# Performance work log

Measured on AMD Instinct MI355X. Metric: run time of the kernel, lower is better.

## Reference

```python
import jax, jax.numpy as jnp
import numpy as np

# DeepSeek-V2 MLA dims (one tensor-parallel shard of 8)
H = 5120          # hidden size
S = 2048          # seq len
B = 1
NH = 16           # 128 heads / 8 devices
Q_LORA = 1536
KV_LORA = 512
NOPE = 128
ROPE = 64
QK = NOPE + ROPE  # 192 per-head q/k dim
VD = 128          # v head dim
DEVICE_NUM = 8
EPS = 1e-6


def rms_norm(x, w):
    v = jnp.mean(jnp.square(x.astype(jnp.float32)), axis=-1, keepdims=True)
    return (x * jax.lax.rsqrt(v + EPS)).astype(x.dtype) * w


def rope_cos_sin(position_ids, dim=ROPE, base=10000.0):
    inv_freq = 1.0 / (base ** (jnp.arange(0, dim, 2, dtype=jnp.float32) / dim))
    freqs = position_ids.astype(jnp.float32)[..., None] * inv_freq       # [B,S,dim/2]
    emb = jnp.concatenate([freqs, freqs], axis=-1)                        # [B,S,dim]
    return jnp.cos(emb), jnp.sin(emb)


def apply_rope(x, cos, sin):
    # DeepSeek interleaved reorder: view(b,h,s,d//2,2).transpose(-1,-2).reshape
    b, h, s, d = x.shape
    x = x.reshape(b, h, s, d // 2, 2).transpose(0, 1, 2, 4, 3).reshape(b, h, s, d)
    x1, x2 = x[..., : d // 2], x[..., d // 2:]
    rot = jnp.concatenate([-x2, x1], axis=-1)
    return x * cos[:, None] + rot * sin[:, None]


def setup_inputs() -> dict:
    key = jax.random.key(0)
    ks = jax.random.split(key, 8)
    sc = 0.02
    hidden_states = jax.random.normal(ks[0], (B, S, H), dtype=jnp.float32)
    position_ids = jnp.arange(S, dtype=jnp.int64 if jax.config.jax_enable_x64 else jnp.int32)[None, :].repeat(B, 0)
    attention_mask = jnp.triu(jnp.full((S, S), -1e9, dtype=jnp.float32), 1)[None, None]
    return {
        "hidden_states": hidden_states,
        "position_ids": position_ids,
        "attention_mask": attention_mask,
        "ln_w": jnp.ones((H,), jnp.float32),
        "q_a_w": jax.random.normal(ks[1], (Q_LORA, H), jnp.float32) * sc,
        "q_a_ln_w": jnp.ones((Q_LORA,), jnp.float32),
        "q_b_w": jax.random.normal(ks[2], (NH * QK, Q_LORA), jnp.float32) * sc,
        "kv_a_w": jax.random.normal(ks[3], (KV_LORA + ROPE, H), jnp.float32) * sc,
        "kv_a_ln_w": jnp.ones((KV_LORA,), jnp.float32),
        "kv_b_w": jax.random.normal(ks[4], (NH * (NOPE + VD), KV_LORA), jnp.float32) * sc,
        "o_w": jax.random.normal(ks[5], (H, NH * VD), jnp.float32) * sc,
    }


def reference(hidden_states, position_ids, attention_mask, ln_w, q_a_w, q_a_ln_w,
              q_b_w, kv_a_w, kv_a_ln_w, kv_b_w, o_w):
    b, s, _ = hidden_states.shape
    residual = hidden_states * (1.0 / DEVICE_NUM)
    x = rms_norm(hidden_states, ln_w)

    # Q path: low-rank down-proj + RMSNorm + up-proj
    q = rms_norm(x @ q_a_w.T, q_a_ln_w) @ q_b_w.T                # [b,s,NH*QK]
    q = q.reshape(b, s, NH, QK).transpose(0, 2, 1, 3)            # [b,NH,s,QK]
    q_nope, q_pe = q[..., :NOPE], q[..., NOPE:]

    # KV path: compressed latent + shared rope key
    ckv = x @ kv_a_w.T                                           # [b,s,KV_LORA+ROPE]
    c_kv, k_pe = ckv[..., :KV_LORA], ckv[..., KV_LORA:]
    k_pe = k_pe.reshape(b, s, 1, ROPE).transpose(0, 2, 1, 3)     # [b,1,s,ROPE]
    kv = rms_norm(c_kv, kv_a_ln_w) @ kv_b_w.T                    # [b,s,NH*(NOPE+VD)]
    kv = kv.reshape(b, s, NH, NOPE + VD).transpose(0, 2, 1, 3)
    k_nope, v = kv[..., :NOPE], kv[..., NOPE:]

    cos, sin = rope_cos_sin(position_ids)
    q_pe = apply_rope(q_pe, cos, sin)
    k_pe = apply_rope(k_pe, cos, sin)

    k = jnp.concatenate([k_nope, jnp.broadcast_to(k_pe, (b, NH, s, ROPE))], axis=-1)
    qf = jnp.concatenate([q_nope, q_pe], axis=-1)

    scores = jnp.einsum('bhqd,bhkd->bhqk', qf, k) * (1.0 / np.sqrt(QK))
    scores = scores + attention_mask
    probs = jax.nn.softmax(scores, axis=-1)
    attn = jnp.einsum('bhqk,bhkd->bhqd', probs, v)               # [b,NH,s,VD]

    out = attn.transpose(0, 2, 1, 3).reshape(b, s, NH * VD) @ o_w.T
    hidden = residual + out
    return hidden.astype(jnp.float32), k.astype(jnp.float32), v.astype(jnp.float32)
```

## Files before the change

### kernel.cpp

```cpp
#include <hip/hip_runtime.h>
#include <math.h>

typedef unsigned short u16;
typedef unsigned int u32;
typedef __attribute__((ext_vector_type(8))) short short8;
typedef __attribute__((ext_vector_type(4))) float f32x4;

#define NHEADS 16
static const int S      = 2048;
static const int Hd     = 5120;
static const int QLORA  = 1536;
static const int KVLORA = 512;
static const int NQK    = 192;
static const int NVD    = 128;
static const int QDIM   = 3072;
static const int KVDIM  = 4096;
static const int NFUSE  = 2176;

__device__ __forceinline__ u16 f2bf(float f) {
    union { float f; u32 u; } v; v.f = f;
    u32 r = v.u + 0x7FFFu + ((v.u >> 16) & 1u);
    return (u16)(r >> 16);
}
__device__ __forceinline__ float bf2f(u16 h) {
    union { u32 u; float f; } v; v.u = (u32)h << 16; return v.f;
}

__global__ void convert_all_kernel(const float* __restrict__ o_w,
                                   const float* __restrict__ q_a_w,
                                   const float* __restrict__ kv_a_w,
                                   const float* __restrict__ q_b_w,
                                   const float* __restrict__ kv_b_w,
                                   u16* __restrict__ o_wb, u16* __restrict__ Wf,
                                   u16* __restrict__ q_b_wb, u16* __restrict__ kv_b_wb) {
    long c = (long)blockIdx.x * 256 + threadIdx.x;
    const float* src; u16* dst; long nsrcc;
    if (c < 2621440L)      { src = o_w;    dst = o_wb;            nsrcc = 2621440L; }
    else if (c < 4587520L) { c -= 2621440L; src = q_a_w; dst = Wf; nsrcc = 1966080L; }
    else if (c < 5406720L) { c -= 4587520L; src = kv_a_w; dst = Wf + 7864320L; nsrcc = 737280L; }
    else if (c < 6586368L) { c -= 5406720L; src = q_b_w;  dst = q_b_wb;  nsrcc = 1179648L; }
    else if (c < 7110656L) { c -= 6586368L; src = kv_b_w; dst = kv_b_wb; nsrcc = 524288L; }
    else return;
    union { u16 h[4]; uint2 u; } p;
    if (c < nsrcc) {
        float4 v = *(const float4*)(src + c * 4);
        p.h[0] = f2bf(v.x); p.h[1] = f2bf(v.y); p.h[2] = f2bf(v.z); p.h[3] = f2bf(v.w);
    } else {
        p.h[0] = p.h[1] = p.h[2] = p.h[3] = 0;
    }
    *(uint2*)(dst + c * 4) = p.u;
}

__global__ void rmsnorm_bf16_kernel(const float* in, const float* __restrict__ w,
                                    u16* out, int D, int in_stride, int out_stride) {
    int row = blockIdx.x;
    const float* x = in + (size_t)row * in_stride;
    u16* y = out + (size_t)row * out_stride;
    float ss = 0.f;
    for (int i = threadIdx.x; i < D; i += blockDim.x) { float v = x[i]; ss += v * v; }
    #pragma unroll
    for (int off = 32; off > 0; off >>= 1) ss += __shfl_xor(ss, off);
    __shared__ float wsum[8];
    int wid = threadIdx.x >> 6, lane = threadIdx.x & 63;
    if (lane == 0) wsum[wid] = ss;
    __syncthreads();
    float tot = 0.f;
    int nw = blockDim.x >> 6;
    for (int i = 0; i < nw; ++i) tot += wsum[i];
    float scale = rsqrtf(tot / (float)D + 1e-6f);
    for (int i = threadIdx.x; i < D; i += blockDim.x) y[i] = f2bf(x[i] * scale * w[i]);
}

__global__ void rms_qkv_kernel(const u16* __restrict__ CF,
                               const float* __restrict__ qw, const float* __restrict__ kw,
                               u16* __restrict__ QAn, u16* __restrict__ CKVN) {
    const int row = blockIdx.x;
    const u16* x; u16* y; const float* w; int D;
    if (blockIdx.y == 0) {
        x = CF + (size_t)row * NFUSE;          y = QAn + (size_t)row * QLORA;
        w = qw; D = QLORA;
    } else {
        x = CF + (size_t)row * NFUSE + QLORA;  y = CKVN + (size_t)row * KVLORA;
        w = kw; D = KVLORA;
    }
    float ss = 0.f;
    for (int i = threadIdx.x; i < D; i += blockDim.x) { float v = bf2f(x[i]); ss += v * v; }
    #pragma unroll
    for (int off = 32; off > 0; off >>= 1) ss += __shfl_xor(ss, off);
    __shared__ float wsum[4];
    int wid = threadIdx.x >> 6, lane = threadIdx.x & 63;
    if (lane == 0) wsum[wid] = ss;
    __syncthreads();
    float tot = wsum[0] + wsum[1] + wsum[2] + wsum[3];
    float scale = rsqrtf(tot / (float)D + 1e-6f);
    for (int i = threadIdx.x; i < D; i += blockDim.x) y[i] = f2bf(bf2f(x[i]) * scale * w[i]);
}

template<int BM, bool SWZ, bool OBF, bool QPERM>
__global__ __launch_bounds__(256) void gemm_k(
    const u16* __restrict__ A, const u16* __restrict__ B, void* __restrict__ Cv,
    int M, int N, int K, const float* __restrict__ resid) {
    constexpr int MR = BM / 32;
    __shared__ u16 As[4][BM * 32];
    __shared__ u16 Bs[4][128 * 32];

    int bm, bn;
    if constexpr (SWZ) {
        const int lin = blockIdx.x + blockIdx.y * gridDim.x;
        const int nwg = gridDim.x * gridDim.y;
        const int xcd = lin & 7, off = lin >> 3;
        const int q = nwg >> 3, r = nwg & 7;
        const int wg = (xcd < r ? xcd * (q + 1) : r * (q + 1) + (xcd - r) * q) + off;
        bm = (wg % gridDim.y) * BM;
        bn = (wg / gridDim.y) * 128;
    } else {
        bm = blockIdx.y * BM;
        bn = blockIdx.x * 128;
    }

    const int tid = threadIdx.x;
    const int w = tid >> 6, lane = tid & 63;
    const int wr = w >> 1, wc = w & 1;
    const int fr = lane & 15, kg = lane >> 4;

    f32x4 acc[MR][4];
    #pragma unroll
    for (int i = 0; i < MR; ++i)
        #pragma unroll
        for (int j = 0; j < 4; ++j) acc[i][j] = (f32x4){0.f, 0.f, 0.f, 0.f};

    const int srow = lane >> 2;
    const int scol = (lane & 3) * 8;
    const u16* Ap0 = A + (size_t)(bm + w * (BM / 4) + srow) * K + scol;
    const u16* Ap1 = Ap0 + (size_t)16 * K;
    const u16* Bp0 = B + (size_t)(bn + w * 32 + srow) * K + scol;
    const u16* Bp1 = Bp0 + (size_t)16 * K;
    const int lda0 = (w * (BM / 4)) * 32;
    const int lda1 = (w * (BM / 4) + 16) * 32;
    const int ldb0 = (w * 32) * 32;
    const int ldb1 = (w * 32 + 16) * 32;

    auto STAGE = [&](int buf, int kk) {
        __builtin_amdgcn_global_load_lds(
            (const __attribute__((address_space(1))) void*)(Ap0 + kk),
            (__attribute__((address_space(3))) void*)&As[buf][lda0], 16, 0, 0);
        if constexpr (BM == 128)
            __builtin_amdgcn_global_load_lds(
                (const __attribute__((address_space(1))) void*)(Ap1 + kk),
                (__attribute__((address_space(3))) void*)&As[buf][lda1], 16, 0, 0);
        __builtin_amdgcn_global_load_lds(
            (const __attribute__((address_space(1))) void*)(Bp0 + kk),
            (__attribute__((address_space(3))) void*)&Bs[buf][ldb0], 16, 0, 0);
        __builtin_amdgcn_global_load_lds(
            (const __attribute__((address_space(1))) void*)(Bp1 + kk),
            (__attribute__((address_space(3))) void*)&Bs[buf][ldb1], 16, 0, 0);
    };
    auto COMP = [&](int buf) {
        short8 af[MR], bfr[4];
        #pragma unroll
        for (int i = 0; i < MR; ++i)
            af[i] = *(const short8*)&As[buf][(wr * (BM / 2) + i * 16 + fr) * 32 + kg * 8];
        #pragma unroll
        for (int i = 0; i < 4; ++i)
            bfr[i] = *(const short8*)&Bs[buf][(wc * 64 + i * 16 + fr) * 32 + kg * 8];
        #pragma unroll
        for (int mi = 0; mi < MR; ++mi)
            #pragma unroll
            for (int ni = 0; ni < 4; ++ni)
                acc[mi][ni] = __builtin_amdgcn_mfma_f32_16x16x32_bf16(af[mi], bfr[ni],
                                                                      acc[mi][ni], 0, 0, 0);
    };

    const int nk = K >> 5;
    STAGE(0, 0);
    STAGE(1, 32);
    for (int kt = 0; kt < nk; ++kt) {
        if (kt + 2 < nk) {
            STAGE((kt + 2) & 3, (kt + 2) << 5);
            if constexpr (BM == 128) asm volatile("s_waitcnt vmcnt(8)" ::: "memory");
            else                     asm volatile("s_waitcnt vmcnt(6)" ::: "memory");
        } else if (kt + 1 < nk) {
            if constexpr (BM == 128) asm volatile("s_waitcnt vmcnt(4)" ::: "memory");
            else                     asm volatile("s_waitcnt vmcnt(3)" ::: "memory");
        } else {
            asm volatile("s_waitcnt vmcnt(0)" ::: "memory");
        }
        __builtin_amdgcn_s_barrier();
        COMP(kt & 3);
    }

    #pragma unroll
    for (int mi = 0; mi < MR; ++mi)
        #pragma unroll
        for (int ni = 0; ni < 4; ++ni)
            #pragma unroll
            for (int r2 = 0; r2 < 4; ++r2) {
                int row = bm + wr * (BM / 2) + mi * 16 + kg * 4 + r2;
                int col = bn + wc * 64 + ni * 16 + fr;
                float v = acc[mi][ni][r2];
                if constexpr (QPERM) {
                    size_t idx = ((size_t)(col / 192) * S + row) * 192 + (col % 192);
                    ((u16*)Cv)[idx] = f2bf(v);
                } else if constexpr (OBF) {
                    ((u16*)Cv)[(size_t)row * N + col] = f2bf(v);
                } else {
                    size_t idx = (size_t)row * N + col;
                    if (resid) v += resid[idx] * 0.125f;
                    ((float*)Cv)[idx] = v;
                }
            }
}

__global__ __launch_bounds__(256) void gemm_qkv_kernel(
    const u16* __restrict__ QAn, const u16* __restrict__ CKVN,
    const u16* __restrict__ q_b_wb, const u16* __restrict__ kv_b_wb,
    u16* __restrict__ Qbf, u16* __restrict__ KVb) {
    __shared__ u16 As[4][64 * 32];
    __shared__ u16 Bs[4][128 * 32];
    const bool isQ = blockIdx.x < 24;
    const u16* A = isQ ? QAn : CKVN;
    const u16* B = isQ ? q_b_wb : kv_b_wb;
    const int K = isQ ? QLORA : KVLORA;
    const int bn = (isQ ? blockIdx.x : blockIdx.x - 24) * 128;
    const int bm = blockIdx.y * 64;

    const int tid = threadIdx.x;
    const int w = tid >> 6, lane = tid & 63;
    const int wr = w >> 1, wc = w & 1;
    const int fr = lane & 15, kg = lane >> 4;

    f32x4 acc[2][4];
    #pragma unroll
    for (int i = 0; i < 2; ++i)
        #pragma unroll
        for (int j = 0; j < 4; ++j) acc[i][j] = (f32x4){0.f, 0.f, 0.f, 0.f};

    const int srow = lane >> 2;
    const int scol = (lane & 3) * 8;
    const u16* Ap0 = A + (size_t)(bm + w * 16 + srow) * K + scol;
    const u16* Bp0 = B + (size_t)(bn + w * 32 + srow) * K + scol;
    const u16* Bp1 = Bp0 + (size_t)16 * K;
    const int lda0 = (w * 16) * 32;
    const int ldb0 = (w * 32) * 32;
    const int ldb1 = (w * 32 + 16) * 32;

    auto STAGE = [&](int buf, int kk) {
        __builtin_amdgcn_global_load_lds(
            (const __attribute__((address_space(1))) void*)(Ap0 + kk),
            (__attribute__((address_space(3))) void*)&As[buf][lda0], 16, 0, 0);
        __builtin_amdgcn_global_load_lds(
            (const __attribute__((address_space(1))) void*)(Bp0 + kk),
            (__attribute__((address_space(3))) void*)&Bs[buf][ldb0], 16, 0, 0);
        __builtin_amdgcn_global_load_lds(
            (const __attribute__((address_space(1))) void*)(Bp1 + kk),
            (__attribute__((address_space(3))) void*)&Bs[buf][ldb1], 16, 0, 0);
    };
    auto COMP = [&](int buf) {
        short8 af[2], bfr[4];
        #pragma unroll
        for (int i = 0; i < 2; ++i)
            af[i] = *(const short8*)&As[buf][(wr * 32 + i * 16 + fr) * 32 + kg * 8];
        #pragma unroll
        for (int i = 0; i < 4; ++i)
            bfr[i] = *(const short8*)&Bs[buf][(wc * 64 + i * 16 + fr) * 32 + kg * 8];
        #pragma unroll
        for (int mi = 0; mi < 2; ++mi)
            #pragma unroll
            for (int ni = 0; ni < 4; ++ni)
                acc[mi][ni] = __builtin_amdgcn_mfma_f32_16x16x32_bf16(af[mi], bfr[ni],
                                                                      acc[mi][ni], 0, 0, 0);
    };

    const int nk = K >> 5;
    STAGE(0, 0);
    STAGE(1, 32);
    for (int kt = 0; kt < nk; ++kt) {
        if (kt + 2 < nk) {
            STAGE((kt + 2) & 3, (kt + 2) << 5);
            asm volatile("s_waitcnt vmcnt(6)" ::: "memory");
        } else if (kt + 1 < nk) {
            asm volatile("s_waitcnt vmcnt(3)" ::: "memory");
        } else {
            asm volatile("s_waitcnt vmcnt(0)" ::: "memory");
        }
        __builtin_amdgcn_s_barrier();
        COMP(kt & 3);
    }

    #pragma unroll
    for (int mi = 0; mi < 2; ++mi)
        #pragma unroll
        for (int ni = 0; ni < 4; ++ni)
            #pragma unroll
            for (int r2 = 0; r2 < 4; ++r2) {
                int row = bm + wr * 32 + mi * 16 + kg * 4 + r2;
                int col = bn + wc * 64 + ni * 16 + fr;
                float v = acc[mi][ni][r2];
                if (isQ) {
                    size_t idx = ((size_t)(col / 192) * S + row) * 192 + (col % 192);
                    Qbf[idx] = f2bf(v);
                } else {
                    KVb[(size_t)row * KVDIM + col] = f2bf(v);
                }
            }
}

__global__ void rope_q_inplace_kernel(u16* __restrict__ Qbf, const int* __restrict__ pos) {
    const int s = blockIdx.x;
    const int t = threadIdx.x;
    const int hh = t >> 5, j = t & 31;
    float ps = (float)pos[s];
    float inv_freq = 1.0f / powf(10000.0f, (float)j * (1.0f / 32.0f));
    float ang = ps * inv_freq;
    float c = cosf(ang), sn = sinf(ang);
    u16* base = Qbf + ((size_t)hh * S + s) * NQK;
    float a = bf2f(base[128 + 2 * j]), b = bf2f(base[128 + 2 * j + 1]);
    __syncthreads();
    base[128 + j] = f2bf(a * c - b * sn);
    base[160 + j] = f2bf(b * c + a * sn);
}

__global__ __launch_bounds__(256) void build_kv64_kernel(
    const u16* __restrict__ KVb, const u16* __restrict__ CF,
    const int* __restrict__ pos_ids,
    float* __restrict__ Kout, float* __restrict__ Vout,
    u16* __restrict__ Kbf, u16* __restrict__ Vtb) {
    const int s0 = blockIdx.x * 64;
    const int h  = blockIdx.y;
    const int t  = threadIdx.x;
    __shared__ u16 T[64][132];

    #pragma unroll
    for (int it = 0; it < 4; ++it) {
        int i = t + it * 256;
        int row = i >> 4, c8 = (i & 15) * 8;
        int s = s0 + row;
        union { uint4 u; u16 hx[8]; } v;
        v.u = *(const uint4*)(KVb + (size_t)s * KVDIM + h * 256 + c8);
        size_t kidx = ((size_t)h * S + s) * NQK + c8;
        *(uint4*)(Kbf + kidx) = v.u;
        float4 f0 = {bf2f(v.hx[0]), bf2f(v.hx[1]), bf2f(v.hx[2]), bf2f(v.hx[3])};
        float4 f1 = {bf2f(v.hx[4]), bf2f(v.hx[5]), bf2f(v.hx[6]), bf2f(v.hx[7])};
        *(float4*)(Kout + kidx) = f0;
        *(float4*)(Kout + kidx + 4) = f1;
    }
    #pragma unroll
    for (int it = 0; it < 4; ++it) {
        int i = t + it * 256;
        int row = i >> 4, c8 = (i & 15) * 8;
        int s = s0 + row;
        union { uint4 u; uint2 d[2]; u16 hx[8]; } v;
        v.u = *(const uint4*)(KVb + (size_t)s * KVDIM + h * 256 + 128 + c8);
        *(uint2*)&T[row][c8]     = v.d[0];
        *(uint2*)&T[row][c8 + 4] = v.d[1];
        size_t vidx = ((size_t)h * S + s) * NVD + c8;
        float4 f0 = {bf2f(v.hx[0]), bf2f(v.hx[1]), bf2f(v.hx[2]), bf2f(v.hx[3])};
        float4 f1 = {bf2f(v.hx[4]), bf2f(v.hx[5]), bf2f(v.hx[6]), bf2f(v.hx[7])};
        *(float4*)(Vout + vidx) = f0;
        *(float4*)(Vout + vidx + 4) = f1;
    }
    #pragma unroll
    for (int it = 0; it < 8; ++it) {
        int i = t + it * 256;
        int row = i >> 5, j = i & 31;
        int s = s0 + row;
        float ps = (float)pos_ids[s];
        float inv_freq = 1.0f / powf(10000.0f, (float)j * (1.0f / 32.0f));
        float ang = ps * inv_freq;
        float c = cosf(ang), sn = sinf(ang);
        u32 pr = *(const u32*)(CF + (size_t)s * NFUSE + QLORA + KVLORA + 2 * j);
        float a = bf2f((u16)pr), b = bf2f((u16)(pr >> 16));
        float k0 = a * c - b * sn;
        float k1 = b * c + a * sn;
        size_t kidx = ((size_t)h * S + s) * NQK;
        Kout[kidx + 128 + j] = k0;
        Kout[kidx + 160 + j] = k1;
        Kbf[kidx + 128 + j] = f2bf(k0);
        Kbf[kidx + 160 + j] = f2bf(k1);
    }
    __syncthreads();
    const int d = t >> 1, half = t & 1;
    #pragma unroll
    for (int c = 0; c < 4; ++c) {
        u16 tmp[8];
        #pragma unroll
        for (int e = 0; e < 8; ++e) tmp[e] = T[half * 32 + c * 8 + e][d];
        *(uint4*)(Vtb + ((size_t)h * NVD + d) * S + s0 + half * 32 + c * 8) = *(uint4*)tmp;
    }
}

__global__ __launch_bounds__(256) void attn_mfma_kernel(
    const u16* __restrict__ Qbf, const u16* __restrict__ Kb,
    const u16* __restrict__ Vtb, u16* __restrict__ ATb) {
    const int h = blockIdx.y;
    const int q0 = (gridDim.x - 1 - blockIdx.x) * 64;
    const int tid = threadIdx.x;
    const int w = tid >> 6, lane = tid & 63;
    const int fr = lane & 15, kg = lane >> 4;

    __shared__ __align__(16) u16 Ks[2][64 * 192];
    __shared__ __align__(16) u16 Vts[2][128 * 64];

    int kSrc[6], vSrc[4];
    #pragma unroll
    for (int i = 0; i < 6; ++i) {
        int D = (w * 6 + i) * 1024 + lane * 16;
        int row = D / 384, wb = D - row * 384;
        kSrc[i] = row * 384 + (wb ^ ((row & 7) << 4));
    }
    #pragma unroll
    for (int i = 0; i < 4; ++i) {
        int D = (w * 4 + i) * 1024 + lane * 16;
        int row = D >> 7, wb = D & 127;
        vSrc[i] = row * (S * 2) + (wb ^ ((row & 7) << 4));
    }
    const char* Kg = (const char*)(Kb + (size_t)h * S * NQK);
    const char* Vg = (const char*)(Vtb + (size_t)h * NVD * S);

    auto STAGE = [&](int buf, int kt) {
        const size_t krow = (size_t)kt * 64;
        #pragma unroll
        for (int i = 0; i < 6; ++i)
            __builtin_amdgcn_global_load_lds(
                (const __attribute__((address_space(1))) void*)(Kg + krow * 384 + kSrc[i]),
                (__attribute__((address_space(3))) void*)((char*)&Ks[buf][0] + (w * 6 + i) * 1024), 16, 0, 0);
        #pragma unroll
        for (int i = 0; i < 4; ++i)
            __builtin_amdgcn_global_load_lds(
                (const __attribute__((address_space(1))) void*)(Vg + krow * 2 + vSrc[i]),
                (__attribute__((address_space(3))) void*)((char*)&Vts[buf][0] + (w * 4 + i) * 1024), 16, 0, 0);
    };

    short8 qf[6];
    {
        const u16* qrow = Qbf + ((size_t)h * S + q0 + w * 16 + fr) * NQK;
        #pragma unroll
        for (int kb = 0; kb < 6; ++kb)
            qf[kb] = *(const short8*)(qrow + kb * 32 + kg * 8);
    }

    f32x4 o[8];
    #pragma unroll
    for (int ni = 0; ni < 8; ++ni) o[ni] = (f32x4){0.f, 0.f, 0.f, 0.f};
    float mrow = -1e30f, lrow = 0.f;
    const float scale = 0.0721687836487032f;
    const int qg = q0 + w * 16 + fr;
    const int swz = (fr & 7) << 4;
    const int nt = (q0 >> 6) + 1;

    STAGE(0, 0);
    asm volatile("s_waitcnt vmcnt(0)" ::: "memory");
    __builtin_amdgcn_s_barrier();

    for (int t = 0; t < nt; ++t) {
        if (t + 1 < nt) STAGE((t + 1) & 1, t + 1);
        const int buf = t & 1;
        const int k0 = t * 64;

        f32x4 sacc[4];
        #pragma unroll
        for (int mi = 0; mi < 4; ++mi) sacc[mi] = (f32x4){0.f, 0.f, 0.f, 0.f};
        __builtin_amdgcn_s_setprio(1);
        #pragma unroll
        for (int mi = 0; mi < 4; ++mi)
            #pragma unroll
            for (int kb = 0; kb < 6; ++kb) {
                const short8 kf = *(const short8*)((const char*)&Ks[buf][0] +
                    (mi * 16 + fr) * 384 + ((kb * 64 + kg * 16) ^ swz));
                sacc[mi] = __builtin_amdgcn_mfma_f32_16x16x32_bf16(kf, qf[kb], sacc[mi], 0, 0, 0);
            }
        __builtin_amdgcn_s_setprio(0);

        const bool diag = (k0 == q0);
        float p[4][4];
        float mx = -1e30f;
        #pragma unroll
        for (int mi = 0; mi < 4; ++mi)
            #pragma unroll
            for (int r = 0; r < 4; ++r) {
                float v = sacc[mi][r] * scale;
                if (diag && (k0 + mi * 16 + kg * 4 + r > qg)) v = -1e30f;
                p[mi][r] = v;
                mx = fmaxf(mx, v);
            }
        mx = fmaxf(mx, __shfl_xor(mx, 16));
        mx = fmaxf(mx, __shfl_xor(mx, 32));
        float mnew = fmaxf(mrow, mx);
        float corr = __expf(mrow - mnew);
        float psum = 0.f;
        #pragma unroll
        for (int mi = 0; mi < 4; ++mi)
            #pragma unroll
            for (int r = 0; r < 4; ++r) {
                float e = __expf(p[mi][r] - mnew);
                p[mi][r] = e;
                psum += e;
            }
        psum += __shfl_xor(psum, 16);
        psum += __shfl_xor(psum, 32);
        lrow = lrow * corr + psum;
        mrow = mnew;
        float corr_r[4];
        #pragma unroll
        for (int r = 0; r < 4; ++r) corr_r[r] = __shfl(corr, kg * 4 + r);
        #pragma unroll
        for (int ni = 0; ni < 8; ++ni) {
            o[ni][0] *= corr_r[0]; o[ni][1] *= corr_r[1];
            o[ni][2] *= corr_r[2]; o[ni][3] *= corr_r[3];
        }

        u32 pk0[4], pk1[4];
        #pragma unroll
        for (int mi = 0; mi < 4; ++mi) {
            pk0[mi] = (u32)f2bf(p[mi][0]) | ((u32)f2bf(p[mi][1]) << 16);
            pk1[mi] = (u32)f2bf(p[mi][2]) | ((u32)f2bf(p[mi][3]) << 16);
        }
        const int srcA = 2 * (kg & 1) * 16 + fr;
        const int srcB = srcA + 16;
        const int hsel = kg >> 1;
        short8 pa[2];
        #pragma unroll
        for (int ks = 0; ks < 2; ++ks) {
            u32 a0 = (u32)__shfl((int)pk0[ks * 2], srcA), b0 = (u32)__shfl((int)pk0[ks * 2 + 1], srcA);
            u32 a1 = (u32)__shfl((int)pk1[ks * 2], srcA), b1 = (u32)__shfl((int)pk1[ks * 2 + 1], srcA);
            u32 a2 = (u32)__shfl((int)pk0[ks * 2], srcB), b2 = (u32)__shfl((int)pk0[ks * 2 + 1], srcB);
            u32 a3 = (u32)__shfl((int)pk1[ks * 2], srcB), b3 = (u32)__shfl((int)pk1[ks * 2 + 1], srcB);
            union { u32 u[4]; short8 s8; } cvt;
            cvt.u[0] = hsel ? b0 : a0;
            cvt.u[1] = hsel ? b1 : a1;
            cvt.u[2] = hsel ? b2 : a2;
            cvt.u[3] = hsel ? b3 : a3;
            pa[ks] = cvt.s8;
        }

        __builtin_amdgcn_s_setprio(1);
        #pragma unroll
        for (int ks = 0; ks < 2; ++ks)
            #pragma unroll
            for (int ni = 0; ni < 8; ++ni) {
                const short8 vf = *(const short8*)((const char*)&Vts[buf][0] +
                    (ni * 16 + fr) * 128 + ((ks * 64 + kg * 16) ^ swz));
                o[ni] = __builtin_amdgcn_mfma_f32_16x16x32_bf16(pa[ks], vf, o[ni], 0, 0, 0);
            }
        __builtin_amdgcn_s_setprio(0);

        asm volatile("s_waitcnt vmcnt(0)" ::: "memory");
        __builtin_amdgcn_s_barrier();
    }

    float inv = 1.f / lrow;
    float inv_r[4];
    #pragma unroll
    for (int r = 0; r < 4; ++r) inv_r[r] = __shfl(inv, kg * 4 + r);
    u16* outp = ATb + (size_t)(q0 + w * 16 + kg * 4) * (NHEADS * NVD) + h * NVD + fr;
    #pragma unroll
    for (int ni = 0; ni < 8; ++ni)
        #pragma unroll
        for (int r = 0; r < 4; ++r)
            outp[(size_t)r * (NHEADS * NVD) + ni * 16] = f2bf(o[ni][r] * inv_r[r]);
}

extern "C" void kernel_launch(void* const* d_in, const int* in_sizes, int n_in,
                              void* d_out, int out_size, void* d_ws, size_t ws_size,
                              hipStream_t stream) {
    (void)in_sizes; (void)n_in; (void)out_size; (void)ws_size;
    const float* hidden    = (const float*)d_in[0];
    const int*   pos       = (const int*)d_in[1];
    const float* ln_w      = (const float*)d_in[3];
    const float* q_a_w     = (const float*)d_in[4];
    const float* q_a_ln_w  = (const float*)d_in[5];
    const float* q_b_w     = (const float*)d_in[6];
    const float* kv_a_w    = (const float*)d_in[7];
    const float* kv_a_ln_w = (const float*)d_in[8];
    const float* kv_b_w    = (const float*)d_in[9];
    const float* o_w       = (const float*)d_in[10];

    float* OUT_H = (float*)d_out;
    float* OUT_K = OUT_H + (size_t)S * Hd;
    float* OUT_V = OUT_K + (size_t)NHEADS * S * NQK;

    char* ws = (char*)d_ws;
    u16*   o_wb    = (u16*)(ws);
    u16*   Wf      = (u16*)(ws + 20971520);
    u16*   Qbf     = (u16*)(ws + 20971520);
    u16*   Vtb     = (u16*)(ws + 33554432);
    u16*   Xb      = (u16*)(ws + 43253760);
    u16*   Kbf     = (u16*)(ws + 43253760);
    u16*   ATb     = (u16*)(ws + 55836672);
    u16*   CF      = (u16*)(ws + 64225280);
    u16*   QAn     = (u16*)(ws + 73138176);
    u16*   CKVN    = (u16*)(ws + 79429632);
    u16*   q_b_wb  = (u16*)(ws + 81526784);
    u16*   kv_b_wb = (u16*)(ws + 90963968);
    u16*   KVb     = (u16*)(ws + 95158272);

    convert_all_kernel<<<27776, 256, 0, stream>>>(o_w, q_a_w, kv_a_w, q_b_w, kv_b_w,
                                                  o_wb, Wf, q_b_wb, kv_b_wb);
    rmsnorm_bf16_kernel<<<S, 256, 0, stream>>>(hidden, ln_w, Xb, Hd, Hd, Hd);
    gemm_k<128, true, true, false><<<dim3(NFUSE / 128, S / 128), 256, 0, stream>>>(Xb, Wf, CF, S, NFUSE, Hd, nullptr);
    rms_qkv_kernel<<<dim3(S, 2), 256, 0, stream>>>(CF, q_a_ln_w, kv_a_ln_w, QAn, CKVN);
    gemm_qkv_kernel<<<dim3(56, S / 64), 256, 0, stream>>>(QAn, CKVN, q_b_wb, kv_b_wb, Qbf, KVb);
    rope_q_inplace_kernel<<<S, 512, 0, stream>>>(Qbf, pos);
    build_kv64_kernel<<<dim3(S / 64, NHEADS), 256, 0, stream>>>(KVb, CF, pos, OUT_K, OUT_V, Kbf, Vtb);
    attn_mfma_kernel<<<dim3(S / 64, NHEADS), 256, 0, stream>>>(Qbf, Kbf, Vtb, ATb);
    gemm_k<64, false, false, false><<<dim3(Hd / 128, S / 64), 256, 0, stream>>>(ATb, o_wb, OUT_H, S, Hd, NHEADS * NVD, hidden);
}
```

Before: 412.3 us.

## Overlap weight conversions with rmsnorm and first GEMM via fused grid kernels

Merges the input rmsnorm with the q_a/kv_a weight conversion into one launch, and folds the o_w/q_b/kv_b weight conversions into extra blocks of a new dedicated first-projection GEMM kernel. The goal is to hide the memory-bound fp32→bf16 conversion traffic behind compute and to cut launch count. The new GEMM uses an XCD-aware block remap and a 4-buffer global_load_lds pipeline. The risk is that the extra conversion blocks compete with GEMM blocks for CUs and bandwidth, and that tile scheduling depends on the block order.

```diff
diff --git a/kernel.cpp b/kernel.cpp
--- a/kernel.cpp
+++ b/kernel.cpp
@@ -26,49 +26,150 @@
     union { u32 u; float f; } v; v.u = (u32)h << 16; return v.f;
 }
 
-__global__ void convert_all_kernel(const float* __restrict__ o_w,
-                                   const float* __restrict__ q_a_w,
-                                   const float* __restrict__ kv_a_w,
-                                   const float* __restrict__ q_b_w,
-                                   const float* __restrict__ kv_b_w,
-                                   u16* __restrict__ o_wb, u16* __restrict__ Wf,
-                                   u16* __restrict__ q_b_wb, u16* __restrict__ kv_b_wb) {
-    long c = (long)blockIdx.x * 256 + threadIdx.x;
-    const float* src; u16* dst; long nsrcc;
-    if (c < 2621440L)      { src = o_w;    dst = o_wb;            nsrcc = 2621440L; }
-    else if (c < 4587520L) { c -= 2621440L; src = q_a_w; dst = Wf; nsrcc = 1966080L; }
-    else if (c < 5406720L) { c -= 4587520L; src = kv_a_w; dst = Wf + 7864320L; nsrcc = 737280L; }
-    else if (c < 6586368L) { c -= 5406720L; src = q_b_w;  dst = q_b_wb;  nsrcc = 1179648L; }
-    else if (c < 7110656L) { c -= 6586368L; src = kv_b_w; dst = kv_b_wb; nsrcc = 524288L; }
-    else return;
-    union { u16 h[4]; uint2 u; } p;
-    if (c < nsrcc) {
-        float4 v = *(const float4*)(src + c * 4);
-        p.h[0] = f2bf(v.x); p.h[1] = f2bf(v.y); p.h[2] = f2bf(v.z); p.h[3] = f2bf(v.w);
+__global__ void prep1_kernel(const float* __restrict__ hidden, const float* __restrict__ ln_w,
+                             const float* __restrict__ q_a_w, const float* __restrict__ kv_a_w,
+                             u16* __restrict__ Xb, u16* __restrict__ Wf) {
+    if (blockIdx.x < 2048) {
+        const int row = blockIdx.x;
+        const float* x = hidden + (size_t)row * Hd;
+        u16* y = Xb + (size_t)row * Hd;
+        float ss = 0.f;
+        for (int i = threadIdx.x; i < Hd; i += 256) { float v = x[i]; ss += v * v; }
+        #pragma unroll
+        for (int off = 32; off > 0; off >>= 1) ss += __shfl_xor(ss, off);
+        __shared__ float wsum[4];
+        int wid = threadIdx.x >> 6, lane = threadIdx.x & 63;
+        if (lane == 0) wsum[wid] = ss;
+        __syncthreads();
+        float tot = wsum[0] + wsum[1] + wsum[2] + wsum[3];
+        float scale = rsqrtf(tot / (float)Hd + 1e-6f);
+        for (int i = threadIdx.x; i < Hd; i += 256) y[i] = f2bf(x[i] * scale * ln_w[i]);
     } else {
-        p.h[0] = p.h[1] = p.h[2] = p.h[3] = 0;
-    }
-    *(uint2*)(dst + c * 4) = p.u;
-}
-
-__global__ void rmsnorm_bf16_kernel(const float* in, const float* __restrict__ w,
-                                    u16* out, int D, int in_stride, int out_stride) {
-    int row = blockIdx.x;
-    const float* x = in + (size_t)row * in_stride;
-    u16* y = out + (size_t)row * out_stride;
-    float ss = 0.f;
-    for (int i = threadIdx.x; i < D; i += blockDim.x) { float v = x[i]; ss += v * v; }
-    #pragma unroll
-    for (int off = 32; off > 0; off >>= 1) ss += __shfl_xor(ss, off);
-    __shared__ float wsum[8];
-    int wid = threadIdx.x >> 6, lane = threadIdx.x & 63;
-    if (lane == 0) wsum[wid] = ss;
-    __syncthreads();
-    float tot = 0.f;
-    int nw = blockDim.x >> 6;
-    for (int i = 0; i < nw; ++i) tot += wsum[i];
-    float scale = rsqrtf(tot / (float)D + 1e-6f);
-    for (int i = threadIdx.x; i < D; i += blockDim.x) y[i] = f2bf(x[i] * scale * w[i]);
+        const long stride = (long)(gridDim.x - 2048) * 256;
+        for (long c0 = (long)(blockIdx.x - 2048) * 256 + threadIdx.x;
+             c0 < 2785280L; c0 += stride) {
+            union { u16 h[4]; uint2 u; } p;
+            if (c0 < 1966080L) {
+                float4 v = *(const float4*)(q_a_w + c0 * 4);
+                p.h[0] = f2bf(v.x); p.h[1] = f2bf(v.y); p.h[2] = f2bf(v.z); p.h[3] = f2bf(v.w);
+                *(uint2*)(Wf + c0 * 4) = p.u;
+            } else {
+                long c = c0 - 1966080L;
+                if (c < 737280L) {
+                    float4 v = *(const float4*)(kv_a_w + c * 4);
+                    p.h[0] = f2bf(v.x); p.h[1] = f2bf(v.y); p.h[2] = f2bf(v.z); p.h[3] = f2bf(v.w);
+                } else {
+                    p.h[0] = p.h[1] = p.h[2] = p.h[3] = 0;
+                }
+                *(uint2*)(Wf + 7864320L + c * 4) = p.u;
+            }
+        }
+    }
+}
+
+__global__ __launch_bounds__(256) void gemm_fusedconv_kernel(
+    const u16* __restrict__ A, const u16* __restrict__ B, u16* __restrict__ C,
+    const float* __restrict__ o_w, const float* __restrict__ q_b_w,
+    const float* __restrict__ kv_b_w,
+    u16* __restrict__ o_wb, u16* __restrict__ q_b_wb, u16* __restrict__ kv_b_wb) {
+    __shared__ u16 As[4][128 * 32];
+    __shared__ u16 Bs[4][128 * 32];
+    if (blockIdx.x >= 272) {
+        const long stride = (long)(gridDim.x - 272) * 256;
+        for (long c0 = (long)(blockIdx.x - 272) * 256 + threadIdx.x;
+             c0 < 4325376L; c0 += stride) {
+            long c = c0; const float* src; u16* dst;
+            if (c < 2621440L)      { src = o_w;    dst = o_wb; }
+            else if (c < 3801088L) { c -= 2621440L; src = q_b_w;  dst = q_b_wb; }
+            else                   { c -= 3801088L; src = kv_b_w; dst = kv_b_wb; }
+            float4 v = *(const float4*)(src + c * 4);
+            u16 p[4] = {f2bf(v.x), f2bf(v.y), f2bf(v.z), f2bf(v.w)};
+            *(uint2*)(dst + c * 4) = *(uint2*)p;
+        }
+        return;
+    }
+    const int K = Hd, N = NFUSE;
+    const int lin = blockIdx.x;
+    const int xcd = lin & 7, off = lin >> 3;
+    const int wg = xcd * 34 + off;
+    const int bm = (wg & 15) * 128;
+    const int bn = (wg >> 4) * 128;
+
+    const int tid = threadIdx.x;
+    const int w = tid >> 6, lane = tid & 63;
+    const int wr = w >> 1, wc = w & 1;
+    const int fr = lane & 15, kg = lane >> 4;
+
+    f32x4 acc[4][4];
+    #pragma unroll
+    for (int i = 0; i < 4; ++i)
+        #pragma unroll
+        for (int j = 0; j < 4; ++j) acc[i][j] = (f32x4){0.f, 0.f, 0.f, 0.f};
+
+    const int srow = lane >> 2;
+    const int scol = (lane & 3) * 8;
+    const u16* Ap0 = A + (size_t)(bm + w * 32 + srow) * K + scol;
+    const u16* Ap1 = Ap0 + (size_t)16 * K;
+    const u16* Bp0 = B + (size_t)(bn + w * 32 + srow) * K + scol;
+    const u16* Bp1 = Bp0 + (size_t)16 * K;
+    const int ld0 = (w * 32) * 32;
+    const int ld1 = (w * 32 + 16) * 32;
+
+    auto STAGE = [&](int buf, int kk) {
+        __builtin_amdgcn_global_load_lds(
+            (const __attribute__((address_space(1))) void*)(Ap0 + kk),
+            (__attribute__((address_space(3))) void*)&As[buf][ld0], 16, 0, 0);
+        __builtin_amdgcn_global_load_lds(
+            (const __attribute__((address_space(1))) void*)(Ap1 + kk),
+            (__attribute__((address_space(3))) void*)&As[buf][ld1], 16, 0, 0);
+        __builtin_amdgcn_global_load_lds(
+            (const __attribute__((address_space(1))) void*)(Bp0 + kk),
+            (__attribute__((address_space(3))) void*)&Bs[buf][ld0], 16, 0, 0);
+        __builtin_amdgcn_global_load_lds(
+            (const __attribute__((address_space(1))) void*)(Bp1 + kk),
+            (__attribute__((address_space(3))) void*)&Bs[buf][ld1], 16, 0, 0);
+    };
+    auto COMP = [&](int buf) {
+        short8 af[4], bfr[4];
+        #pragma unroll
+        for (int i = 0; i < 4; ++i) {
+            af[i]  = *(const short8*)&As[buf][(wr * 64 + i * 16 + fr) * 32 + kg * 8];
+            bfr[i] = *(const short8*)&Bs[buf][(wc * 64 + i * 16 + fr) * 32 + kg * 8];
+        }
+        #pragma unroll
+        for (int mi = 0; mi < 4; ++mi)
+            #pragma unroll
+            for (int ni = 0; ni < 4; ++ni)
+                acc[mi][ni] = __builtin_amdgcn_mfma_f32_16x16x32_bf16(af[mi], bfr[ni],
+                                                                      acc[mi][ni], 0, 0, 0);
+    };
+
+    const int nk = K >> 5;
+    STAGE(0, 0);
+    STAGE(1, 32);
+    for (int kt = 0; kt < nk; ++kt) {
+        if (kt + 2 < nk) {
+            STAGE((kt + 2) & 3, (kt + 2) << 5);
+            asm volatile("s_waitcnt vmcnt(8)" ::: "memory");
+        } else if (kt + 1 < nk) {
+            asm volatile("s_waitcnt vmcnt(4)" ::: "memory");
+        } else {
+            asm volatile("s_waitcnt vmcnt(0)" ::: "memory");
+        }
+        __builtin_amdgcn_s_barrier();
+        COMP(kt & 3);
+    }
+
+    #pragma unroll
+    for (int mi = 0; mi < 4; ++mi)
+        #pragma unroll
+        for (int ni = 0; ni < 4; ++ni)
+            #pragma unroll
+            for (int r2 = 0; r2 < 4; ++r2) {
+                int row = bm + wr * 64 + mi * 16 + kg * 4 + r2;
+                int col = bn + wc * 64 + ni * 16 + fr;
+                C[(size_t)row * N + col] = f2bf(acc[mi][ni][r2]);
+            }
 }
 
 __global__ void rms_qkv_kernel(const u16* __restrict__ CF,
@@ -594,10 +695,9 @@
     u16*   kv_b_wb = (u16*)(ws + 90963968);
     u16*   KVb     = (u16*)(ws + 95158272);
 
-    convert_all_kernel<<<27776, 256, 0, stream>>>(o_w, q_a_w, kv_a_w, q_b_w, kv_b_w,
-                                                  o_wb, Wf, q_b_wb, kv_b_wb);
-    rmsnorm_bf16_kernel<<<S, 256, 0, stream>>>(hidden, ln_w, Xb, Hd, Hd, Hd);
-    gemm_k<128, true, true, false><<<dim3(NFUSE / 128, S / 128), 256, 0, stream>>>(Xb, Wf, CF, S, NFUSE, Hd, nullptr);
+    prep1_kernel<<<3072, 256, 0, stream>>>(hidden, ln_w, q_a_w, kv_a_w, Xb, Wf);
+    gemm_fusedconv_kernel<<<1296, 256, 0, stream>>>(Xb, Wf, CF, o_w, q_b_w, kv_b_w,
+                                                    o_wb, q_b_wb, kv_b_wb);
     rms_qkv_kernel<<<dim3(S, 2), 256, 0, stream>>>(CF, q_a_ln_w, kv_a_ln_w, QAn, CKVN);
     gemm_qkv_kernel<<<dim3(56, S / 64), 256, 0, stream>>>(QAn, CKVN, q_b_wb, kv_b_wb, Qbf, KVb);
     rope_q_inplace_kernel<<<S, 512, 0, stream>>>(Qbf, pos);
```

Result: slower. 440.2 us (+6.8%).

## Use K=64 tiles with XOR-swizzled LDS and double buffering in GEMMs

Applied to the files above, without the earlier changes.

Replaces the 4-stage K=32 GEMM pipeline with a 2-buffer K=64 pipeline. Each stage loads rows as 128-byte chunks whose 16-byte columns are XOR-swizzled by row, so the MFMA fragment reads from LDS avoid bank conflicts. This halves the number of barriers per K step and is meant to cut LDS conflict stalls. In exchange the prefetch depth drops to one stage, with a full vmcnt(0) wait every iteration, so global memory latency may be less well hidden. The unused QPERM path is removed.

```diff
diff --git a/kernel.cpp b/kernel.cpp
--- a/kernel.cpp
+++ b/kernel.cpp
@@ -96,13 +96,14 @@
     for (int i = threadIdx.x; i < D; i += blockDim.x) y[i] = f2bf(bf2f(x[i]) * scale * w[i]);
 }
 
-template<int BM, bool SWZ, bool OBF, bool QPERM>
-__global__ __launch_bounds__(256) void gemm_k(
+template<int BM, bool SWZ, bool OBF>
+__global__ __launch_bounds__(256) void gemm64_k(
     const u16* __restrict__ A, const u16* __restrict__ B, void* __restrict__ Cv,
     int M, int N, int K, const float* __restrict__ resid) {
     constexpr int MR = BM / 32;
-    __shared__ u16 As[4][BM * 32];
-    __shared__ u16 Bs[4][128 * 32];
+    constexpr int ALOADS = (BM * 128) / 4096;
+    __shared__ u16 As[2][BM * 64];
+    __shared__ u16 Bs[2][128 * 64];
 
     int bm, bn;
     if constexpr (SWZ) {
@@ -122,6 +123,7 @@
     const int w = tid >> 6, lane = tid & 63;
     const int wr = w >> 1, wc = w & 1;
     const int fr = lane & 15, kg = lane >> 4;
+    const int swz = (fr & 7) << 4;
 
     f32x4 acc[MR][4];
     #pragma unroll
@@ -129,64 +131,62 @@
         #pragma unroll
         for (int j = 0; j < 4; ++j) acc[i][j] = (f32x4){0.f, 0.f, 0.f, 0.f};
 
-    const int srow = lane >> 2;
-    const int scol = (lane & 3) * 8;
-    const u16* Ap0 = A + (size_t)(bm + w * (BM / 4) + srow) * K + scol;
-    const u16* Ap1 = Ap0 + (size_t)16 * K;
-    const u16* Bp0 = B + (size_t)(bn + w * 32 + srow) * K + scol;
-    const u16* Bp1 = Bp0 + (size_t)16 * K;
-    const int lda0 = (w * (BM / 4)) * 32;
-    const int lda1 = (w * (BM / 4) + 16) * 32;
-    const int ldb0 = (w * 32) * 32;
-    const int ldb1 = (w * 32 + 16) * 32;
-
-    auto STAGE = [&](int buf, int kk) {
-        __builtin_amdgcn_global_load_lds(
-            (const __attribute__((address_space(1))) void*)(Ap0 + kk),
-            (__attribute__((address_space(3))) void*)&As[buf][lda0], 16, 0, 0);
-        if constexpr (BM == 128)
+    const size_t K2 = (size_t)K * 2;
+
+    auto STAGE = [&](int buf, int kt) {
+        const char* ga = (const char*)A + ((size_t)bm * K + (size_t)kt * 64) * 2;
+        const char* gb = (const char*)B + ((size_t)bn * K + (size_t)kt * 64) * 2;
+        #pragma unroll
+        for (int j = 0; j < ALOADS; ++j) {
+            const int D = j * 4096 + tid * 16;
+            const int r = D >> 7, c = (D & 127) ^ ((r & 7) << 4);
             __builtin_amdgcn_global_load_lds(
-                (const __attribute__((address_space(1))) void*)(Ap1 + kk),
-                (__attribute__((address_space(3))) void*)&As[buf][lda1], 16, 0, 0);
-        __builtin_amdgcn_global_load_lds(
-            (const __attribute__((address_space(1))) void*)(Bp0 + kk),
-            (__attribute__((address_space(3))) void*)&Bs[buf][ldb0], 16, 0, 0);
-        __builtin_amdgcn_global_load_lds(
-            (const __attribute__((address_space(1))) void*)(Bp1 + kk),
-            (__attribute__((address_space(3))) void*)&Bs[buf][ldb1], 16, 0, 0);
+                (const __attribute__((address_space(1))) void*)(ga + (size_t)r * K2 + c),
+                (__attribute__((address_space(3))) void*)((char*)&As[buf][0] + D), 16, 0, 0);
+        }
+        #pragma unroll
+        for (int j = 0; j < 4; ++j) {
+            const int D = j * 4096 + tid * 16;
+            const int r = D >> 7, c = (D & 127) ^ ((r & 7) << 4);
+            __builtin_amdgcn_global_load_lds(
+                (const __attribute__((address_space(1))) void*)(gb + (size_t)r * K2 + c),
+                (__attribute__((address_space(3))) void*)((char*)&Bs[buf][0] + D), 16, 0, 0);
+        }
     };
     auto COMP = [&](int buf) {
-        short8 af[MR], bfr[4];
-        #pragma unroll
-        for (int i = 0; i < MR; ++i)
-            af[i] = *(const short8*)&As[buf][(wr * (BM / 2) + i * 16 + fr) * 32 + kg * 8];
-        #pragma unroll
-        for (int i = 0; i < 4; ++i)
-            bfr[i] = *(const short8*)&Bs[buf][(wc * 64 + i * 16 + fr) * 32 + kg * 8];
-        #pragma unroll
-        for (int mi = 0; mi < MR; ++mi)
-            #pragma unroll
-            for (int ni = 0; ni < 4; ++ni)
-                acc[mi][ni] = __builtin_amdgcn_mfma_f32_16x16x32_bf16(af[mi], bfr[ni],
-                                                                      acc[mi][ni], 0, 0, 0);
+        #pragma unroll
+        for (int s = 0; s < 2; ++s) {
+            short8 af[MR], bfr[4];
+            #pragma unroll
+            for (int i = 0; i < MR; ++i) {
+                const int row = wr * (BM / 2) + i * 16 + fr;
+                af[i] = *(const short8*)((const char*)&As[buf][0] +
+                         row * 128 + ((s * 64 + kg * 16) ^ swz));
+            }
+            #pragma unroll
+            for (int i = 0; i < 4; ++i) {
+                const int row = wc * 64 + i * 16 + fr;
+                bfr[i] = *(const short8*)((const char*)&Bs[buf][0] +
+                          row * 128 + ((s * 64 + kg * 16) ^ swz));
+            }
+            #pragma unroll
+            for (int mi = 0; mi < MR; ++mi)
+                #pragma unroll
+                for (int ni = 0; ni < 4; ++ni)
+                    acc[mi][ni] = __builtin_amdgcn_mfma_f32_16x16x32_bf16(
+                        af[mi], bfr[ni], acc[mi][ni], 0, 0, 0);
+        }
     };
 
-    const int nk = K >> 5;
+    const int nk = K >> 6;
     STAGE(0, 0);
-    STAGE(1, 32);
+    asm volatile("s_waitcnt vmcnt(0)" ::: "memory");
+    __builtin_amdgcn_s_barrier();
     for (int kt = 0; kt < nk; ++kt) {
-        if (kt + 2 < nk) {
-            STAGE((kt + 2) & 3, (kt + 2) << 5);
-            if constexpr (BM == 128) asm volatile("s_waitcnt vmcnt(8)" ::: "memory");
-            else                     asm volatile("s_waitcnt vmcnt(6)" ::: "memory");
-        } else if (kt + 1 < nk) {
-            if constexpr (BM == 128) asm volatile("s_waitcnt vmcnt(4)" ::: "memory");
-            else                     asm volatile("s_waitcnt vmcnt(3)" ::: "memory");
-        } else {
-            asm volatile("s_waitcnt vmcnt(0)" ::: "memory");
-        }
+        if (kt + 1 < nk) STAGE((kt + 1) & 1, kt + 1);
+        COMP(kt & 1);
+        asm volatile("s_waitcnt vmcnt(0)" ::: "memory");
         __builtin_amdgcn_s_barrier();
-        COMP(kt & 3);
     }
 
     #pragma unroll
@@ -197,14 +197,11 @@
             for (int r2 = 0; r2 < 4; ++r2) {
                 int row = bm + wr * (BM / 2) + mi * 16 + kg * 4 + r2;
                 int col = bn + wc * 64 + ni * 16 + fr;
+                size_t idx = (size_t)row * N + col;
                 float v = acc[mi][ni][r2];
-                if constexpr (QPERM) {
-                    size_t idx = ((size_t)(col / 192) * S + row) * 192 + (col % 192);
+                if constexpr (OBF) {
                     ((u16*)Cv)[idx] = f2bf(v);
-                } else if constexpr (OBF) {
-                    ((u16*)Cv)[(size_t)row * N + col] = f2bf(v);
                 } else {
-                    size_t idx = (size_t)row * N + col;
                     if (resid) v += resid[idx] * 0.125f;
                     ((float*)Cv)[idx] = v;
                 }
@@ -597,11 +594,11 @@
     convert_all_kernel<<<27776, 256, 0, stream>>>(o_w, q_a_w, kv_a_w, q_b_w, kv_b_w,
                                                   o_wb, Wf, q_b_wb, kv_b_wb);
     rmsnorm_bf16_kernel<<<S, 256, 0, stream>>>(hidden, ln_w, Xb, Hd, Hd, Hd);
-    gemm_k<128, true, true, false><<<dim3(NFUSE / 128, S / 128), 256, 0, stream>>>(Xb, Wf, CF, S, NFUSE, Hd, nullptr);
+    gemm64_k<128, true, true><<<dim3(NFUSE / 128, S / 128), 256, 0, stream>>>(Xb, Wf, CF, S, NFUSE, Hd, nullptr);
     rms_qkv_kernel<<<dim3(S, 2), 256, 0, stream>>>(CF, q_a_ln_w, kv_a_ln_w, QAn, CKVN);
     gemm_qkv_kernel<<<dim3(56, S / 64), 256, 0, stream>>>(QAn, CKVN, q_b_wb, kv_b_wb, Qbf, KVb);
     rope_q_inplace_kernel<<<S, 512, 0, stream>>>(Qbf, pos);
     build_kv64_kernel<<<dim3(S / 64, NHEADS), 256, 0, stream>>>(KVb, CF, pos, OUT_K, OUT_V, Kbf, Vtb);
     attn_mfma_kernel<<<dim3(S / 64, NHEADS), 256, 0, stream>>>(Qbf, Kbf, Vtb, ATb);
-    gemm_k<64, false, false, false><<<dim3(Hd / 128, S / 64), 256, 0, stream>>>(ATb, o_wb, OUT_H, S, Hd, NHEADS * NVD, hidden);
-}
+    gemm64_k<64, false, false><<<dim3(Hd / 128, S / 64), 256, 0, stream>>>(ATb, o_wb, OUT_H, S, Hd, NHEADS * NVD, hidden);
+}
```

Result: faster. 386.6 us (-6.2%).
